# Kernel optimization log

Hardware: AMD Instinct MI355X
Metric: run time of the kernel (lower is better)

## Reference

```python
import jax, jax.numpy as jnp
import numpy as np
import math
from jax import lax

TSCALE = 256
NUM_SAMPLE = 32
PERBIN = 3
WINDOWS = [4, 8, 16, 32, 64, 128, 192, 256]
RATIO = 0.25
B = 2
DIM = 512
H1 = 256   # hid_dim_1d
H3 = 512   # hid_dim_3d
H2 = 128   # hid_dim_2d


def _bin_mask(xmin, xmax, tscale, num_sample, perbin):
    # exact replica of BEM._get_interp1d_bin_mask (setup-time numpy)
    plen = float(xmax - xmin)
    step = plen / (num_sample * perbin - 1.0)
    samples = [xmin + step * i for i in range(num_sample * perbin)]
    cols = []
    for idx in range(num_sample):
        v = np.zeros([tscale])
        for s in samples[idx * perbin:(idx + 1) * perbin]:
            up = math.ceil(s)
            dec, down = math.modf(s)
            if 0 <= int(down) <= tscale - 1:
                v[int(down)] += 1 - dec
            if 0 <= int(up) <= tscale - 1:
                v[int(up)] += dec
        cols.append(v / perbin)
    return np.stack(cols, axis=1)  # (tscale, num_sample)


def build_sample_mask():
    mats = []
    for w in WINDOWS:
        ws = w + w * RATIO
        vecs = []
        for t in range(TSCALE):
            d = ws * 0.5
            vecs.append(_bin_mask(t - d, t + d, TSCALE, NUM_SAMPLE, PERBIN))
        mats.append(np.stack(vecs, axis=2))  # (T, N, T)
    m = np.stack(mats, axis=3).astype(np.float32)  # (T, N, T, W)
    return jnp.asarray(m.reshape(TSCALE, -1))  # (T, N*T*W)


def gn(x, g, b, groups=32, eps=1e-5):
    Bsz, C = x.shape[0], x.shape[1]
    xr = x.reshape(Bsz, groups, -1)
    mu = xr.mean(-1, keepdims=True)
    var = xr.var(-1, keepdims=True)
    xr = (xr - mu) * lax.rsqrt(var + eps)
    x = xr.reshape(x.shape)
    bshape = (1, C) + (1,) * (x.ndim - 2)
    return x * g.reshape(bshape) + b.reshape(bshape)


def conv(x, w, b, strides, padding, dn):
    y = lax.conv_general_dilated(x, w, strides, padding, dimension_numbers=dn)
    return y + b.reshape((1, -1) + (1,) * (y.ndim - 2))


def setup_inputs() -> dict:
    key = jax.random.key(0)
    ks = jax.random.split(key, 16)

    def w(k, shape, fan):
        return (jax.random.normal(k, shape) * (1.0 / np.sqrt(fan))).astype(jnp.float32)

    inp = {}
    inp['x'] = jax.random.normal(ks[0], (B, DIM, TSCALE), jnp.float32)
    inp['sample_mask'] = build_sample_mask()
    inp['c1_w'] = w(ks[1], (H1, DIM, 3), DIM * 3)
    inp['c1_b'] = jnp.zeros((H1,), jnp.float32)
    inp['gn1_g'] = jnp.ones((H1,), jnp.float32)
    inp['gn1_b'] = jnp.zeros((H1,), jnp.float32)
    inp['r3d_w'] = w(ks[2], (H3, H1, NUM_SAMPLE, 1, 1), H1 * NUM_SAMPLE)
    inp['r3d_b'] = jnp.zeros((H3,), jnp.float32)
    inp['gn3_g'] = jnp.ones((H3,), jnp.float32)
    inp['gn3_b'] = jnp.zeros((H3,), jnp.float32)
    inp['r2d_w'] = w(ks[3], (H2, H3, 1, 1), H3)
    inp['r2d_b'] = jnp.zeros((H2,), jnp.float32)
    inp['gn2_g'] = jnp.ones((H2,), jnp.float32)
    inp['gn2_b'] = jnp.zeros((H2,), jnp.float32)
    inp['s1_w'] = w(ks[4], (H2, H2, 3, 3), H2 * 9)
    inp['s1_b'] = jnp.zeros((H2,), jnp.float32)
    inp['sgn_g'] = jnp.ones((H2,), jnp.float32)
    inp['sgn_b'] = jnp.zeros((H2,), jnp.float32)
    inp['s2_w'] = w(ks[5], (1, H2, 1, 1), H2)
    inp['s2_b'] = jnp.zeros((1,), jnp.float32)
    inp['e1_w'] = w(ks[6], (H2, H2, 3, 3), H2 * 9)
    inp['e1_b'] = jnp.zeros((H2,), jnp.float32)
    inp['egn_g'] = jnp.ones((H2,), jnp.float32)
    inp['egn_b'] = jnp.zeros((H2,), jnp.float32)
    inp['e2_w'] = w(ks[7], (1, H2, 1, 1), H2)
    inp['e2_b'] = jnp.zeros((1,), jnp.float32)
    return inp


def reference(x, sample_mask, c1_w, c1_b, gn1_g, gn1_b, r3d_w, r3d_b, gn3_g, gn3_b,
              r2d_w, r2d_b, gn2_g, gn2_b, s1_w, s1_b, sgn_g, sgn_b, s2_w, s2_b,
              e1_w, e1_b, egn_g, egn_b, e2_w, e2_b):
    relu = jax.nn.relu
    W = len(WINDOWS)
    # conv_1: Unit1D(k=3, same pad) + GN + ReLU  -> (B, H1, T)
    h = relu(gn(conv(x, c1_w, c1_b, (1,), [(1, 1)], ('NCH', 'OIH', 'NCH')), gn1_g, gn1_b))
    Bsz, C, T = h.shape
    # sample: dense GEMM against sparse interp1d mask -> (B, C, N, T, W)
    samp = jnp.matmul(h, sample_mask).reshape(Bsz, C, NUM_SAMPLE, T, W)
    # reduction_layer 'fc': Conv3d over the N axis (kernel=stride=N) + GN + ReLU
    y = conv(samp, r3d_w, r3d_b, (NUM_SAMPLE, 1, 1), 'VALID', ('NCDHW', 'OIDHW', 'NCDHW'))
    y = relu(gn(y, gn3_g, gn3_b))[:, :, 0]  # squeeze depth -> (B, H3, T, W)
    f = relu(gn(conv(y, r2d_w, r2d_b, (1, 1), 'VALID', ('NCHW', 'OIHW', 'NCHW')), gn2_g, gn2_b))

    def head(w1, b1, gg, gb, w2, b2):
        t = relu(gn(conv(f, w1, b1, (1, 1), [(1, 1), (1, 1)], ('NCHW', 'OIHW', 'NCHW')), gg, gb))
        return jax.nn.sigmoid(conv(t, w2, b2, (1, 1), 'VALID', ('NCHW', 'OIHW', 'NCHW')))

    cs = head(s1_w, s1_b, sgn_g, sgn_b, s2_w, s2_b)  # (B,1,T,W)
    ce = head(e1_w, e1_b, egn_g, egn_b, e2_w, e2_b)  # (B,1,T,W)
    return jnp.concatenate([cs, ce], axis=1)  # (B,2,T,W): [start, end]
```

## Files before the change

### kernel.cpp

```cpp
#include <hip/hip_runtime.h>
#include <hip/hip_bf16.h>

typedef __hip_bfloat16 bf16;
typedef __attribute__((ext_vector_type(8))) short short8;
typedef __attribute__((ext_vector_type(4))) float f32x4;

static __device__ __forceinline__ float b2f(bf16 v) { return __bfloat162float(v); }

static __device__ __forceinline__ float ldin(const void* p, long i, int bf) {
    return bf ? b2f(((const bf16*)p)[i]) : ((const float*)p)[i];
}

__global__ void detect_k(const unsigned short* __restrict__ x16, int* __restrict__ flag) {
    __shared__ int cnt[256];
    unsigned short u = x16[threadIdx.x];
    int e = (u >> 7) & 0xFF;
    cnt[threadIdx.x] = (e >= 100 && e <= 140) ? 1 : 0;
    __syncthreads();
    for (int off = 128; off > 0; off >>= 1) {
        if (threadIdx.x < off) cnt[threadIdx.x] += cnt[threadIdx.x + off];
        __syncthreads();
    }
    if (threadIdx.x == 0) *flag = (cnt[0] > 217) ? 1 : 0;
}

__global__ void transpose_w_k(const void* __restrict__ in, float* __restrict__ out,
                              int M, int K, const int* __restrict__ flagp) {
    int bf = *flagp;
    int idx = blockIdx.x * 256 + threadIdx.x;
    if (idx >= M * K) return;
    int k = idx / M, m = idx - k * M;
    out[idx] = ldin(in, (long)m * K + k, bf);
}

__global__ __launch_bounds__(256) void transpose_w3b_k(const void* __restrict__ w3,
                                                       bf16* __restrict__ out,
                                                       const int* __restrict__ flagp) {
    int bf = *flagp;
    int h3 = blockIdx.x;
    __shared__ bf16 t[8192];
    long base = (long)h3 * 8192;
    for (int i = threadIdx.x; i < 8192; i += 256)
        t[i] = __float2bfloat16(ldin(w3, base + i, bf));
    __syncthreads();
    for (int i = threadIdx.x; i < 8192; i += 256) {
        int n = i >> 8, c = i & 255;
        out[((long)n * 512 + h3) * 256 + c] = t[c * 32 + n];
    }
}

__global__ void cast_hT_k(const float* __restrict__ h, bf16* __restrict__ out) {
    int idx = blockIdx.x * 256 + threadIdx.x;
    if (idx >= 131072) return;
    int b = idx >> 16, r = idx & 65535;
    int tau = r >> 8, c = r & 255;
    out[idx] = __float2bfloat16(h[b * 65536 + c * 256 + tau]);
}

__global__ void im2col_x_k(const void* __restrict__ x, float* __restrict__ colx,
                           const int* __restrict__ flagp) {
    int bf = *flagp;
    int idx = blockIdx.x * 256 + threadIdx.x;
    if (idx >= 786432) return;
    int t = idx & 255;
    int b = idx / 393216;
    int k = (idx - b * 393216) >> 8;
    int c = k / 3, q = k - c * 3;
    int tt = t + q - 1;
    colx[idx] = (tt >= 0 && tt < 256) ? ldin(x, ((long)b * 512 + c) * 256 + tt, bf) : 0.f;
}

__global__ void im2col_f_k(const float* __restrict__ f, float* __restrict__ col) {
    int idx = blockIdx.x * 256 + threadIdx.x;
    if (idx >= 4718592) return;
    int p = idx & 2047;
    int rem = idx >> 11;
    int b = rem / 1152;
    int k = rem - b * 1152;
    int c = k / 9, q = k - c * 9;
    int dy = q / 3, dx = q - dy * 3;
    int t = p >> 3, w = p & 7;
    int tt = t + dy - 1, ww = w + dx - 1;
    col[idx] = (tt >= 0 && tt < 256 && ww >= 0 && ww < 8)
                   ? f[((long)b * 128 + c) * 2048 + tt * 8 + ww] : 0.f;
}

__global__ __launch_bounds__(256) void pgemm_mfma(
    const bf16* __restrict__ w3b, const bf16* __restrict__ hbT,
    float* __restrict__ P)
{
    int z = blockIdx.z;
    int b = z >> 5, n = z & 31;
    int bm = blockIdx.y;
    int tid = threadIdx.x;
    int wv = tid >> 6, lane = tid & 63;
    int q = lane >> 4, col = lane & 15;

    f32x4 acc[16];
    #pragma unroll
    for (int i = 0; i < 16; ++i) acc[i] = (f32x4){0.f, 0.f, 0.f, 0.f};

    const short8* Abase = (const short8*)(w3b + ((long)n * 512 + bm * 64 + wv * 16 + col) * 256);
    const short8* Bbase = (const short8*)(hbT + (long)b * 65536);

    #pragma unroll
    for (int kc = 0; kc < 8; ++kc) {
        short8 af = Abase[kc * 4 + q];
        #pragma unroll
        for (int nt = 0; nt < 16; ++nt) {
            short8 bfr = Bbase[(nt * 16 + col) * 32 + kc * 4 + q];
            acc[nt] = __builtin_amdgcn_mfma_f32_16x16x32_bf16(af, bfr, acc[nt], 0, 0, 0);
        }
    }

    long dbase = (long)b * 4194304 + (long)n * 256 +
                 (long)(bm * 64 + wv * 16 + q * 4) * 8192 + col;
    #pragma unroll
    for (int nt = 0; nt < 16; ++nt)
        #pragma unroll
        for (int r = 0; r < 4; ++r)
            P[dbase + (long)r * 8192 + nt * 16] = acc[nt][r];
}

template<int BM, int BP, int TM, int TP>
__global__ __launch_bounds__(256) void gemm_t(
    const float* __restrict__ A, const float* __restrict__ B, float* __restrict__ C,
    const void* __restrict__ bias, const void* __restrict__ bias2,
    int M, int K, int P, int az_mod, int bz_div,
    long a_zs, long b_zs, long c_zs1, long c_zs2, int c_ms,
    int zmod, int ksplit, long sstride, int accum, const int* __restrict__ flagp)
{
    int bf = *flagp;
    int zraw = blockIdx.z;
    int z = zraw % zmod;
    int ks = zraw / zmod;
    int klen = K / ksplit;
    int kbeg = ks * klen;
    int kend = kbeg + klen;
    int za = z % az_mod;
    const float* A2 = A + (long)za * a_zs;
    const float* B2 = B + (long)(z / bz_div) * b_zs;
    float* C2 = C + (long)(z / bz_div) * c_zs1 + (long)za * c_zs2;
    const void* bi = (bias2 != nullptr && za != 0) ? bias2 : bias;

    __shared__ float As[16][BM];
    __shared__ float Bs[16][BP];
    int tid = threadIdx.x;
    int ty = tid >> 4, tx = tid & 15;
    int lk = tid >> 4;
    int lma = (tid & 15) * TM;
    int lpb = (tid & 15) * TP;
    int m0 = blockIdx.y * BM, p0 = blockIdx.x * BP;

    float acc[TM][TP];
    #pragma unroll
    for (int i = 0; i < TM; ++i)
        #pragma unroll
        for (int j = 0; j < TP; ++j) acc[i][j] = 0.f;

    float ra[TM], rb[TP];
    {
        const float* ap = A2 + (long)(kbeg + lk) * M + m0 + lma;
        const float* bp = B2 + (long)(kbeg + lk) * P + p0 + lpb;
        #pragma unroll
        for (int u = 0; u < TM; ++u) ra[u] = ap[u];
        #pragma unroll
        for (int u = 0; u < TP; ++u) rb[u] = bp[u];
    }

    for (int kc = kbeg; kc < kend; kc += 16) {
        #pragma unroll
        for (int u = 0; u < TM; ++u) As[lk][lma + u] = ra[u];
        #pragma unroll
        for (int u = 0; u < TP; ++u) Bs[lk][lpb + u] = rb[u];
        __syncthreads();
        if (kc + 16 < kend) {
            const float* ap = A2 + (long)(kc + 16 + lk) * M + m0 + lma;
            const float* bp = B2 + (long)(kc + 16 + lk) * P + p0 + lpb;
            #pragma unroll
            for (int u = 0; u < TM; ++u) ra[u] = ap[u];
            #pragma unroll
            for (int u = 0; u < TP; ++u) rb[u] = bp[u];
        }
        #pragma unroll
        for (int kk = 0; kk < 16; ++kk) {
            float av[TM], bv[TP];
            #pragma unroll
            for (int i = 0; i < TM; ++i) av[i] = As[kk][ty * TM + i];
            #pragma unroll
            for (int j = 0; j < TP; ++j) bv[j] = Bs[kk][tx * TP + j];
            #pragma unroll
            for (int i = 0; i < TM; ++i)
                #pragma unroll
                for (int j = 0; j < TP; ++j)
                    acc[i][j] += av[i] * bv[j];
        }
        __syncthreads();
    }

    #pragma unroll
    for (int i = 0; i < TM; ++i) {
        int m = m0 + ty * TM + i;
        float bb = bi ? ldin(bi, m, bf) : 0.f;
        #pragma unroll
        for (int j = 0; j < TP; ++j) {
            long idx = (long)m * c_ms + p0 + tx * TP + j;
            if (accum == 1) C2[sstride * ks + idx] = acc[i][j];
            else if (accum == 2) C2[idx] += acc[i][j];
            else C2[idx] = acc[i][j] + bb;
        }
    }
}

__global__ __launch_bounds__(256) void gemm_q(
    const float* __restrict__ A, const float* __restrict__ B, float* __restrict__ C,
    const void* __restrict__ bias, const void* __restrict__ bias2,
    int M, int K, int P, int az_mod, int bz_div,
    long a_zs, long b_zs, long c_zs1, long c_zs2, int c_ms,
    int zmod, int ksplit, long sstride, int accum, const int* __restrict__ flagp)
{
    int bf = *flagp;
    int zraw = blockIdx.z;
    int z = zraw % zmod;
    int ks = zraw / zmod;
    int klen = K / ksplit;
    int kbeg = ks * klen, kend = kbeg + klen;
    int za = z % az_mod;
    const float* A2 = A + (long)za * a_zs;
    const float* B2 = B + (long)(z / bz_div) * b_zs;
    float* C2 = C + (long)(z / bz_div) * c_zs1 + (long)za * c_zs2;
    const void* bi = (bias2 != nullptr && za != 0) ? bias2 : bias;

    __shared__ float As[16][128];
    __shared__ float Bs[16][128];
    int tid = threadIdx.x;
    int ty = tid >> 4, tx = tid & 15;
    int lk = tid >> 4;
    int lc4 = (tid & 15) * 4;
    int m0 = blockIdx.y * 128, p0 = blockIdx.x * 128;

    float acc[8][8];
    #pragma unroll
    for (int i = 0; i < 8; ++i)
        #pragma unroll
        for (int j = 0; j < 8; ++j) acc[i][j] = 0.f;

    float4 ra0, ra1, rb0, rb1;
    {
        const float* ap = A2 + (long)(kbeg + lk) * M + m0 + lc4;
        const float* bp = B2 + (long)(kbeg + lk) * P + p0 + lc4;
        ra0 = *(const float4*)ap;  ra1 = *(const float4*)(ap + 64);
        rb0 = *(const float4*)bp;  rb1 = *(const float4*)(bp + 64);
    }

    for (int kc = kbeg; kc < kend; kc += 16) {
        *(float4*)&As[lk][lc4]      = ra0;
        *(float4*)&As[lk][64 + lc4] = ra1;
        *(float4*)&Bs[lk][lc4]      = rb0;
        *(float4*)&Bs[lk][64 + lc4] = rb1;
        __syncthreads();
        if (kc + 16 < kend) {
            const float* ap = A2 + (long)(kc + 16 + lk) * M + m0 + lc4;
            const float* bp = B2 + (long)(kc + 16 + lk) * P + p0 + lc4;
            ra0 = *(const float4*)ap;  ra1 = *(const float4*)(ap + 64);
            rb0 = *(const float4*)bp;  rb1 = *(const float4*)(bp + 64);
        }
        #pragma unroll
        for (int kk = 0; kk < 16; ++kk) {
            float4 av0 = *(float4*)&As[kk][ty * 4];
            float4 av1 = *(float4*)&As[kk][64 + ty * 4];
            float4 bv0 = *(float4*)&Bs[kk][tx * 4];
            float4 bv1 = *(float4*)&Bs[kk][64 + tx * 4];
            float av[8] = {av0.x, av0.y, av0.z, av0.w, av1.x, av1.y, av1.z, av1.w};
            float bv[8] = {bv0.x, bv0.y, bv0.z, bv0.w, bv1.x, bv1.y, bv1.z, bv1.w};
            #pragma unroll
            for (int i = 0; i < 8; ++i)
                #pragma unroll
                for (int j = 0; j < 8; ++j)
                    acc[i][j] += av[i] * bv[j];
        }
        __syncthreads();
    }

    #pragma unroll
    for (int r = 0; r < 2; ++r)
        #pragma unroll
        for (int i = 0; i < 4; ++i) {
            int m = m0 + r * 64 + ty * 4 + i;
            float bb = bi ? ldin(bi, m, bf) : 0.f;
            #pragma unroll
            for (int c = 0; c < 2; ++c)
                #pragma unroll
                for (int j = 0; j < 4; ++j) {
                    long idx = (long)m * c_ms + p0 + c * 64 + tx * 4 + j;
                    float v = acc[r * 4 + i][c * 4 + j];
                    if (accum == 1) C2[sstride * ks + idx] = v;
                    else if (accum == 2) C2[idx] += v;
                    else C2[idx] = v + bb;
                }
        }
}

__global__ void reduce_k(const float* __restrict__ bufs, float* __restrict__ out,
                         int n4, int ns, long sstride, const void* __restrict__ b1,
                         const void* __restrict__ b2, int rshift, int cshift, int cmask,
                         const int* __restrict__ flagp)
{
    int bf = *flagp;
    int i = blockIdx.x * 256 + threadIdx.x;
    if (i >= n4) return;
    long e = (long)i * 4;
    float4 s = *(const float4*)(bufs + e);
    for (int k = 1; k < ns; ++k) {
        float4 v = *(const float4*)(bufs + (long)k * sstride + e);
        s.x += v.x; s.y += v.y; s.z += v.z; s.w += v.w;
    }
    const void* bp = (rshift >= 0 && ((e >> rshift) & 3) >= 2) ? b2 : b1;
    int c = (int)((e >> cshift) & cmask);
    float bb = ldin(bp, c, bf);
    *(float4*)(out + e) = make_float4(s.x + bb, s.y + bb, s.z + bb, s.w + bb);
}

__global__ __launch_bounds__(1024) void gn_relu_k(
    float* __restrict__ buf, const void* __restrict__ g, const void* __restrict__ bt,
    int C, int S, int groups, const int* __restrict__ flagp)
{
    int bf = *flagp;
    int nt = blockDim.x;
    int gid = blockIdx.x;
    int b = gid / groups, gr = gid % groups;
    int cpg = C / groups;
    long cnt = (long)cpg * S;
    float* base = buf + ((long)b * C + (long)gr * cpg) * S;
    double s = 0.0, s2 = 0.0;
    for (long i = threadIdx.x; i < cnt; i += nt) {
        float v = base[i];
        s += v; s2 += (double)v * v;
    }
    __shared__ double rs[1024], rq[1024];
    rs[threadIdx.x] = s; rq[threadIdx.x] = s2;
    __syncthreads();
    for (int off = nt >> 1; off > 0; off >>= 1) {
        if (threadIdx.x < off) { rs[threadIdx.x] += rs[threadIdx.x + off]; rq[threadIdx.x] += rq[threadIdx.x + off]; }
        __syncthreads();
    }
    double mean_d = rs[0] / (double)cnt;
    float mean = (float)mean_d;
    float var = (float)(rq[0] / (double)cnt - mean_d * mean_d);
    float rstd = rsqrtf(var + 1e-5f);
    for (long i = threadIdx.x; i < cnt; i += nt) {
        int c = gr * cpg + (int)(i / S);
        float v = (base[i] - mean) * rstd * ldin(g, c, bf) + ldin(bt, c, bf);
        base[i] = v > 0.f ? v : 0.f;
    }
}

__global__ __launch_bounds__(384) void build_table_k(
    const void* __restrict__ mask, int* __restrict__ tabd,
    float* __restrict__ tabw, const int* __restrict__ flagp)
{
    int bf = *flagp;
    int nw = blockIdx.x;
    int w = nw >> 5, n = nw & 31;
    int tid = threadIdx.x;
    int d = tid - 165;
    float v = 0.f;
    if (d <= 165) {
        if (d < 0) v = ldin(mask, (long)(254 + d) * 65536 + ((long)n * 256 + 254) * 8 + w, bf);
        else       v = ldin(mask, (long)(1 + d) * 65536 + ((long)n * 256 + 1) * 8 + w, bf);
    }
    __shared__ unsigned char nz[384];
    nz[tid] = (v != 0.f) ? 1 : 0;
    if (tid < 6) { tabd[nw * 6 + tid] = 0; tabw[nw * 6 + tid] = 0.f; }
    __syncthreads();
    if (v != 0.f) {
        int slot = 0;
        for (int j = 0; j < tid; ++j) slot += nz[j];
        if (slot < 6) { tabd[nw * 6 + slot] = d; tabw[nw * 6 + slot] = v; }
    }
}

__global__ void build_corr_k(const void* __restrict__ mask, const int* __restrict__ tabd,
                             const float* __restrict__ tabw, float* __restrict__ corrB,
                             const int* __restrict__ flagp) {
    int bf = *flagp;
    int idx = blockIdx.x * 256 + threadIdx.x;
    if (idx >= 65536) return;
    int n = idx >> 11, p = idx & 2047;
    int t = p >> 3, w = p & 7;
    float mv = ldin(mask, ((long)n * 256 + t) * 8 + w, bf);
    float sub = 0.f;
    int base = (w * 32 + n) * 6;
    for (int k = 0; k < 6; ++k)
        if (tabd[base + k] == -t && tabw[base + k] != 0.f) sub += tabw[base + k];
    corrB[idx] = mv - sub;
}

__global__ void p0t_k(const float* __restrict__ P, float* __restrict__ p0t) {
    int idx = blockIdx.x * 256 + threadIdx.x;
    if (idx >= 32768) return;
    int h3 = idx & 511, n = (idx >> 9) & 31, b = idx >> 14;
    p0t[idx] = P[(((long)(b * 512 + h3) * 32) + n) * 256];
}

__global__ __launch_bounds__(256) void apply_y_k(
    const float* __restrict__ P, const int* __restrict__ tabd,
    const float* __restrict__ tabw, const void* __restrict__ r3b,
    float* __restrict__ y, const int* __restrict__ flagp)
{
    int bf = *flagp;
    int h3 = blockIdx.x;
    __shared__ float2 Pl2[8192];
    __shared__ float4 Tp4[768];
    const float4* p04 = (const float4*)(P + (long)h3 * 8192);
    const float4* p14 = (const float4*)(P + (512L + h3) * 8192);
    float4* pl4 = (float4*)Pl2;
    for (int i = threadIdx.x; i < 2048; i += 256) {
        float4 a = p04[i], b = p14[i];
        pl4[i * 2]     = make_float4(a.x, b.x, a.y, b.y);
        pl4[i * 2 + 1] = make_float4(a.z, b.z, a.w, b.w);
    }
    float2* tp2 = (float2*)Tp4;
    for (int i = threadIdx.x; i < 1536; i += 256)
        tp2[i] = make_float2(tabw[i], __int_as_float(tabd[i]));
    __syncthreads();

    int t = threadIdx.x;
    float a0[8], a1[8];
    #pragma unroll
    for (int w = 0; w < 8; ++w) { a0[w] = 0.f; a1[w] = 0.f; }

    #pragma unroll 1
    for (int n = 0; n < 32; ++n) {
        const float2* Pn = Pl2 + (n << 8);
        #pragma unroll
        for (int w = 0; w < 8; ++w) {
            int e4 = ((w << 5) + n) * 3;
            float4 q0 = Tp4[e4], q1 = Tp4[e4 + 1], q2 = Tp4[e4 + 2];
            float wts[6] = {q0.x, q0.z, q1.x, q1.z, q2.x, q2.z};
            int   dss[6] = {__float_as_int(q0.y), __float_as_int(q0.w),
                            __float_as_int(q1.y), __float_as_int(q1.w),
                            __float_as_int(q2.y), __float_as_int(q2.w)};
            #pragma unroll
            for (int k = 0; k < 6; ++k) {
                int tau = t + dss[k];
                int idx = tau & 255;
                float wt = ((unsigned)tau < 256u) ? wts[k] : 0.f;
                float2 pv = Pn[idx];
                a0[w] += wt * pv.x;
                a1[w] += wt * pv.y;
            }
        }
    }

    float bias = ldin(r3b, h3, bf);
    long y0 = (long)h3 * 2048 + (long)t * 8;
    long y1 = y0 + 512L * 2048;
    *(float4*)(y + y0)     = make_float4(a0[0] + bias, a0[1] + bias, a0[2] + bias, a0[3] + bias);
    *(float4*)(y + y0 + 4) = make_float4(a0[4] + bias, a0[5] + bias, a0[6] + bias, a0[7] + bias);
    *(float4*)(y + y1)     = make_float4(a1[0] + bias, a1[1] + bias, a1[2] + bias, a1[3] + bias);
    *(float4*)(y + y1 + 4) = make_float4(a1[4] + bias, a1[5] + bias, a1[6] + bias, a1[7] + bias);
}

__global__ void head_out_k(const float* __restrict__ t1s, const float* __restrict__ t1e,
                           const void* __restrict__ s2w, const void* __restrict__ s2b,
                           const void* __restrict__ e2w, const void* __restrict__ e2b,
                           void* __restrict__ out, const int* __restrict__ flagp) {
    int bf = *flagp;
    int idx = blockIdx.x * 256 + threadIdx.x;
    if (idx >= 4096) return;
    int b = idx >> 11, p = idx & 2047;
    const float* ts = t1s + (long)b * 262144 + p;
    const float* te = t1e + (long)b * 262144 + p;
    float as = ldin(s2b, 0, bf), ae = ldin(e2b, 0, bf);
    #pragma unroll 8
    for (int c = 0; c < 128; ++c) {
        as += ldin(s2w, c, bf) * ts[(long)c * 2048];
        ae += ldin(e2w, c, bf) * te[(long)c * 2048];
    }
    float vs = 1.f / (1.f + expf(-as));
    float ve = 1.f / (1.f + expf(-ae));
    long o0 = ((long)b * 2) * 2048 + p;
    long o1 = ((long)b * 2 + 1) * 2048 + p;
    if (bf) {
        ((bf16*)out)[o0] = __float2bfloat16(vs);
        ((bf16*)out)[o1] = __float2bfloat16(ve);
    } else {
        ((float*)out)[o0] = vs;
        ((float*)out)[o1] = ve;
    }
}

extern "C" void kernel_launch(void* const* d_in, const int* in_sizes, int n_in,
                              void* d_out, int out_size, void* d_ws, size_t ws_size,
                              hipStream_t stream) {
    const void* x    = d_in[0];
    const void* mask = d_in[1];
    const void* c1w  = d_in[2];
    const void* c1b  = d_in[3];
    const void* gn1g = d_in[4];
    const void* gn1b = d_in[5];
    const void* w3   = d_in[6];
    const void* r3b  = d_in[7];
    const void* gn3g = d_in[8];
    const void* gn3b = d_in[9];
    const void* w2   = d_in[10];
    const void* r2b  = d_in[11];
    const void* gn2g = d_in[12];
    const void* gn2b = d_in[13];
    const void* s1w  = d_in[14];
    const void* s1b  = d_in[15];
    const void* sgng = d_in[16];
    const void* sgnb = d_in[17];
    const void* s2w  = d_in[18];
    const void* s2b  = d_in[19];
    const void* e1w  = d_in[20];
    const void* e1b  = d_in[21];
    const void* egng = d_in[22];
    const void* egnb = d_in[23];
    const void* e2w  = d_in[24];
    const void* e2b  = d_in[25];
    float* ws = (float*)d_ws;

    int*   flagI = (int*)(ws + 0);
    float* h     = ws + 64;
    float* c1t   = ws + 131136;
    float* w2t   = ws + 524352;
    float* s1t   = ws + 589888;
    float* e1t   = ws + 737344;
    float* corrB = ws + 884800;
    float* tabw  = ws + 950336;
    int*   tabd  = (int*)(ws + 951872);
    float* p0t   = ws + 953408;
    float* t1s   = ws + 986176;
    float* t1e   = ws + 1510464;
    float* f     = ws + 2034752;
    float* y     = ws + 2559040;
    float* w3reg = ws + 4656192;
    float* Pb    = ws + 8850496;
    bf16*  w3b   = (bf16*)w3reg;
    bf16*  hbT   = (bf16*)(w3reg + 2097152);
    float* colx  = Pb;
    float* col   = Pb;
    float* bufs_c1 = y;
    float* bufs_r2 = Pb;
    float* bufs_hd = y;

    dim3 blk(256);
    dim3 blkG(1024);

    detect_k<<<dim3(1), blk, 0, stream>>>((const unsigned short*)x, flagI);

    transpose_w_k<<<dim3(1536), blk, 0, stream>>>(c1w, c1t, 256, 1536, flagI);
    transpose_w_k<<<dim3(256),  blk, 0, stream>>>(w2,  w2t, 128, 512, flagI);
    transpose_w_k<<<dim3(576),  blk, 0, stream>>>(s1w, s1t, 128, 1152, flagI);
    transpose_w_k<<<dim3(576),  blk, 0, stream>>>(e1w, e1t, 128, 1152, flagI);
    transpose_w3b_k<<<dim3(512), blk, 0, stream>>>(w3, w3b, flagI);
    build_table_k<<<dim3(256), dim3(384), 0, stream>>>(mask, tabd, tabw, flagI);
    build_corr_k<<<dim3(256), blk, 0, stream>>>(mask, tabd, tabw, corrB, flagI);

    im2col_x_k<<<dim3(3072), blk, 0, stream>>>(x, colx, flagI);
    gemm_t<64,64,4,4><<<dim3(4,4,16), blk, 0, stream>>>(
        c1t, colx, bufs_c1, nullptr, nullptr, 256, 1536, 256,
        1, 1, 0L, 393216L, 65536L, 0L, 256, 2, 8, 131072L, 1, flagI);
    reduce_k<<<dim3(128), blk, 0, stream>>>(bufs_c1, h, 32768, 8, 131072L,
                                            c1b, nullptr, -1, 8, 255, flagI);
    gn_relu_k<<<dim3(64), blkG, 0, stream>>>(h, gn1g, gn1b, 256, 256, 32, flagI);

    cast_hT_k<<<dim3(512), blk, 0, stream>>>(h, hbT);
    pgemm_mfma<<<dim3(1, 8, 64), blk, 0, stream>>>(w3b, hbT, Pb);

    apply_y_k<<<dim3(512), blk, 0, stream>>>(Pb, tabd, tabw, r3b, y, flagI);
    p0t_k<<<dim3(128), blk, 0, stream>>>(Pb, p0t);
    gemm_t<64,64,4,4><<<dim3(32,8,2), blk, 0, stream>>>(
        p0t, corrB, y, nullptr, nullptr, 512, 32, 2048,
        2, 1, 16384L, 0L, 0L, 1048576L, 2048, 2, 1, 0L, 2, flagI);
    gn_relu_k<<<dim3(64), blkG, 0, stream>>>(y, gn3g, gn3b, 512, 2048, 32, flagI);

    gemm_t<64,64,4,4><<<dim3(32,2,8), blk, 0, stream>>>(
        w2t, y, bufs_r2, nullptr, nullptr, 128, 512, 2048,
        1, 1, 0L, 1048576L, 262144L, 0L, 2048, 2, 4, 524288L, 1, flagI);
    reduce_k<<<dim3(512), blk, 0, stream>>>(bufs_r2, f, 131072, 4, 524288L,
                                            r2b, nullptr, -1, 11, 127, flagI);
    gn_relu_k<<<dim3(64), blkG, 0, stream>>>(f, gn2g, gn2b, 128, 2048, 32, flagI);

    im2col_f_k<<<dim3(18432), blk, 0, stream>>>(f, col);
    gemm_q<<<dim3(16,1,24), blk, 0, stream>>>(
        s1t, col, bufs_hd, nullptr, nullptr, 128, 1152, 2048,
        2, 2, 147456L, 2359296L, 262144L, 524288L, 2048, 4, 6, 1048576L, 1, flagI);
    reduce_k<<<dim3(1024), blk, 0, stream>>>(bufs_hd, t1s, 262144, 6, 1048576L,
                                             s1b, e1b, 18, 11, 127, flagI);
    gn_relu_k<<<dim3(64), blkG, 0, stream>>>(t1s, sgng, sgnb, 128, 2048, 32, flagI);
    gn_relu_k<<<dim3(64), blkG, 0, stream>>>(t1e, egng, egnb, 128, 2048, 32, flagI);

    head_out_k<<<dim3(16), blk, 0, stream>>>(t1s, t1e, s2w, s2b, e2w, e2b, d_out, flagI);
}
```

Baseline: 463.1 us.

## Move conv1 and head 3x3 convs to bf16 MFMA GEMMs with k-major im2col

The conv1 and both head 3x3 convolutions now run through a new bf16 MFMA GEMM kernel that reads operands directly from global memory. Weights are cast to bf16 without transposing, and the im2col buffers are written as bf16 in a K-contiguous layout. This removes the fp32 SIMT GEMMs along with their split-K partial buffers and reduce passes, with bias added in the GEMM epilogue. In exchange, operands are rounded to bf16, and the new kernel has no LDS staging, so it depends on global/L2 reuse and launches relatively few blocks.

```diff
diff --git a/kernel.cpp b/kernel.cpp
--- a/kernel.cpp
+++ b/kernel.cpp
@@ -24,6 +24,14 @@
     if (threadIdx.x == 0) *flag = (cnt[0] > 217) ? 1 : 0;
 }
 
+__global__ void cast_bf_k(const void* __restrict__ in, bf16* __restrict__ out,
+                          int n, const int* __restrict__ flagp) {
+    int bf = *flagp;
+    int idx = blockIdx.x * 256 + threadIdx.x;
+    if (idx >= n) return;
+    out[idx] = __float2bfloat16(ldin(in, idx, bf));
+}
+
 __global__ void transpose_w_k(const void* __restrict__ in, float* __restrict__ out,
                               int M, int K, const int* __restrict__ flagp) {
     int bf = *flagp;
@@ -57,32 +65,78 @@
     out[idx] = __float2bfloat16(h[b * 65536 + c * 256 + tau]);
 }
 
-__global__ void im2col_x_k(const void* __restrict__ x, float* __restrict__ colx,
-                           const int* __restrict__ flagp) {
+__global__ void im2col_xb_k(const void* __restrict__ x, bf16* __restrict__ out,
+                            const int* __restrict__ flagp) {
     int bf = *flagp;
     int idx = blockIdx.x * 256 + threadIdx.x;
     if (idx >= 786432) return;
-    int t = idx & 255;
     int b = idx / 393216;
-    int k = (idx - b * 393216) >> 8;
+    int rem = idx - b * 393216;
+    int t = rem / 1536, k = rem - t * 1536;
     int c = k / 3, q = k - c * 3;
     int tt = t + q - 1;
-    colx[idx] = (tt >= 0 && tt < 256) ? ldin(x, ((long)b * 512 + c) * 256 + tt, bf) : 0.f;
-}
-
-__global__ void im2col_f_k(const float* __restrict__ f, float* __restrict__ col) {
+    float v = (tt >= 0 && tt < 256) ? ldin(x, ((long)b * 512 + c) * 256 + tt, bf) : 0.f;
+    out[idx] = __float2bfloat16(v);
+}
+
+__global__ void im2col_fb_k(const float* __restrict__ f, bf16* __restrict__ out) {
     int idx = blockIdx.x * 256 + threadIdx.x;
     if (idx >= 4718592) return;
-    int p = idx & 2047;
-    int rem = idx >> 11;
-    int b = rem / 1152;
-    int k = rem - b * 1152;
+    int b = idx / 2359296;
+    int rem = idx - b * 2359296;
+    int p = rem / 1152, k = rem - p * 1152;
     int c = k / 9, q = k - c * 9;
     int dy = q / 3, dx = q - dy * 3;
     int t = p >> 3, w = p & 7;
     int tt = t + dy - 1, ww = w + dx - 1;
-    col[idx] = (tt >= 0 && tt < 256 && ww >= 0 && ww < 8)
-                   ? f[((long)b * 128 + c) * 2048 + tt * 8 + ww] : 0.f;
+    float v = (tt >= 0 && tt < 256 && ww >= 0 && ww < 8)
+                  ? f[((long)b * 128 + c) * 2048 + tt * 8 + ww] : 0.f;
+    out[idx] = __float2bfloat16(v);
+}
+
+template<int NT>
+__global__ __launch_bounds__(256) void wgemm_mfma(
+    const bf16* __restrict__ A, const bf16* __restrict__ B, float* __restrict__ C,
+    const void* __restrict__ bias1, const void* __restrict__ bias2,
+    int M, int K, int P, int a_div, long a_zs, const int* __restrict__ flagp)
+{
+    int bf = *flagp;
+    int z = blockIdx.z;
+    const bf16* A2 = A + (long)(z / a_div) * a_zs;
+    const bf16* B2 = B + (long)(z & 1) * (long)P * K;
+    float* C2 = C + (long)z * M * P;
+    const void* bi = (z / a_div) ? bias2 : bias1;
+
+    int tid = threadIdx.x;
+    int wv = tid >> 6, lane = tid & 63;
+    int q = lane >> 4, col = lane & 15;
+    int m0 = blockIdx.y * 64 + wv * 16;
+    int p0 = blockIdx.x * (16 * NT);
+
+    f32x4 acc[NT];
+    #pragma unroll
+    for (int i = 0; i < NT; ++i) acc[i] = (f32x4){0.f, 0.f, 0.f, 0.f};
+
+    const short8* Ab = (const short8*)(A2 + (long)(m0 + col) * K);
+    int kch = K >> 5;
+    for (int kc = 0; kc < kch; ++kc) {
+        short8 af = Ab[kc * 4 + q];
+        #pragma unroll
+        for (int nt = 0; nt < NT; ++nt) {
+            const short8* Bb = (const short8*)(B2 + (long)(p0 + nt * 16 + col) * K);
+            short8 bfr = Bb[kc * 4 + q];
+            acc[nt] = __builtin_amdgcn_mfma_f32_16x16x32_bf16(af, bfr, acc[nt], 0, 0, 0);
+        }
+    }
+
+    float bv[4];
+    #pragma unroll
+    for (int r = 0; r < 4; ++r) bv[r] = ldin(bi, m0 + q * 4 + r, bf);
+    #pragma unroll
+    for (int nt = 0; nt < NT; ++nt)
+        #pragma unroll
+        for (int r = 0; r < 4; ++r)
+            C2[(long)(m0 + q * 4 + r) * P + p0 + nt * 16 + col] = acc[nt][r] + bv[r];
 }
 
 __global__ __launch_bounds__(256) void pgemm_mfma(
@@ -210,95 +264,6 @@
             else C2[idx] = acc[i][j] + bb;
         }
     }
-}
-
-__global__ __launch_bounds__(256) void gemm_q(
-    const float* __restrict__ A, const float* __restrict__ B, float* __restrict__ C,
-    const void* __restrict__ bias, const void* __restrict__ bias2,
-    int M, int K, int P, int az_mod, int bz_div,
-    long a_zs, long b_zs, long c_zs1, long c_zs2, int c_ms,
-    int zmod, int ksplit, long sstride, int accum, const int* __restrict__ flagp)
-{
-    int bf = *flagp;
-    int zraw = blockIdx.z;
-    int z = zraw % zmod;
-    int ks = zraw / zmod;
-    int klen = K / ksplit;
-    int kbeg = ks * klen, kend = kbeg + klen;
-    int za = z % az_mod;
-    const float* A2 = A + (long)za * a_zs;
-    const float* B2 = B + (long)(z / bz_div) * b_zs;
-    float* C2 = C + (long)(z / bz_div) * c_zs1 + (long)za * c_zs2;
-    const void* bi = (bias2 != nullptr && za != 0) ? bias2 : bias;
-
-    __shared__ float As[16][128];
-    __shared__ float Bs[16][128];
-    int tid = threadIdx.x;
-    int ty = tid >> 4, tx = tid & 15;
-    int lk = tid >> 4;
-    int lc4 = (tid & 15) * 4;
-    int m0 = blockIdx.y * 128, p0 = blockIdx.x * 128;
-
-    float acc[8][8];
-    #pragma unroll
-    for (int i = 0; i < 8; ++i)
-        #pragma unroll
-        for (int j = 0; j < 8; ++j) acc[i][j] = 0.f;
-
-    float4 ra0, ra1, rb0, rb1;
-    {
-        const float* ap = A2 + (long)(kbeg + lk) * M + m0 + lc4;
-        const float* bp = B2 + (long)(kbeg + lk) * P + p0 + lc4;
-        ra0 = *(const float4*)ap;  ra1 = *(const float4*)(ap + 64);
-        rb0 = *(const float4*)bp;  rb1 = *(const float4*)(bp + 64);
-    }
-
-    for (int kc = kbeg; kc < kend; kc += 16) {
-        *(float4*)&As[lk][lc4]      = ra0;
-        *(float4*)&As[lk][64 + lc4] = ra1;
-        *(float4*)&Bs[lk][lc4]      = rb0;
-        *(float4*)&Bs[lk][64 + lc4] = rb1;
-        __syncthreads();
-        if (kc + 16 < kend) {
-            const float* ap = A2 + (long)(kc + 16 + lk) * M + m0 + lc4;
-            const float* bp = B2 + (long)(kc + 16 + lk) * P + p0 + lc4;
-            ra0 = *(const float4*)ap;  ra1 = *(const float4*)(ap + 64);
-            rb0 = *(const float4*)bp;  rb1 = *(const float4*)(bp + 64);
-        }
-        #pragma unroll
-        for (int kk = 0; kk < 16; ++kk) {
-            float4 av0 = *(float4*)&As[kk][ty * 4];
-            float4 av1 = *(float4*)&As[kk][64 + ty * 4];
-            float4 bv0 = *(float4*)&Bs[kk][tx * 4];
-            float4 bv1 = *(float4*)&Bs[kk][64 + tx * 4];
-            float av[8] = {av0.x, av0.y, av0.z, av0.w, av1.x, av1.y, av1.z, av1.w};
-            float bv[8] = {bv0.x, bv0.y, bv0.z, bv0.w, bv1.x, bv1.y, bv1.z, bv1.w};
-            #pragma unroll
-            for (int i = 0; i < 8; ++i)
-                #pragma unroll
-                for (int j = 0; j < 8; ++j)
-                    acc[i][j] += av[i] * bv[j];
-        }
-        __syncthreads();
-    }
-
-    #pragma unroll
-    for (int r = 0; r < 2; ++r)
-        #pragma unroll
-        for (int i = 0; i < 4; ++i) {
-            int m = m0 + r * 64 + ty * 4 + i;
-            float bb = bi ? ldin(bi, m, bf) : 0.f;
-            #pragma unroll
-            for (int c = 0; c < 2; ++c)
-                #pragma unroll
-                for (int j = 0; j < 4; ++j) {
-                    long idx = (long)m * c_ms + p0 + c * 64 + tx * 4 + j;
-                    float v = acc[r * 4 + i][c * 4 + j];
-                    if (accum == 1) C2[sstride * ks + idx] = v;
-                    else if (accum == 2) C2[idx] += v;
-                    else C2[idx] = v + bb;
-                }
-        }
 }
 
 __global__ void reduce_k(const float* __restrict__ bufs, float* __restrict__ out,
@@ -527,7 +492,6 @@
     float* c1t   = ws + 131136;
     float* w2t   = ws + 524352;
     float* s1t   = ws + 589888;
-    float* e1t   = ws + 737344;
     float* corrB = ws + 884800;
     float* tabw  = ws + 950336;
     int*   tabd  = (int*)(ws + 951872);
@@ -540,31 +504,28 @@
     float* Pb    = ws + 8850496;
     bf16*  w3b   = (bf16*)w3reg;
     bf16*  hbT   = (bf16*)(w3reg + 2097152);
-    float* colx  = Pb;
-    float* col   = Pb;
-    float* bufs_c1 = y;
+    bf16*  c1wb  = (bf16*)c1t;
+    bf16*  hwb   = (bf16*)s1t;
+    bf16*  colxb = (bf16*)y;
+    bf16*  fcolb = (bf16*)Pb;
     float* bufs_r2 = Pb;
-    float* bufs_hd = y;
 
     dim3 blk(256);
     dim3 blkG(1024);
 
     detect_k<<<dim3(1), blk, 0, stream>>>((const unsigned short*)x, flagI);
 
-    transpose_w_k<<<dim3(1536), blk, 0, stream>>>(c1w, c1t, 256, 1536, flagI);
-    transpose_w_k<<<dim3(256),  blk, 0, stream>>>(w2,  w2t, 128, 512, flagI);
-    transpose_w_k<<<dim3(576),  blk, 0, stream>>>(s1w, s1t, 128, 1152, flagI);
-    transpose_w_k<<<dim3(576),  blk, 0, stream>>>(e1w, e1t, 128, 1152, flagI);
+    cast_bf_k<<<dim3(1536), blk, 0, stream>>>(c1w, c1wb, 393216, flagI);
+    cast_bf_k<<<dim3(576),  blk, 0, stream>>>(s1w, hwb, 147456, flagI);
+    cast_bf_k<<<dim3(576),  blk, 0, stream>>>(e1w, hwb + 147456, 147456, flagI);
+    transpose_w_k<<<dim3(256), blk, 0, stream>>>(w2, w2t, 128, 512, flagI);
     transpose_w3b_k<<<dim3(512), blk, 0, stream>>>(w3, w3b, flagI);
     build_table_k<<<dim3(256), dim3(384), 0, stream>>>(mask, tabd, tabw, flagI);
     build_corr_k<<<dim3(256), blk, 0, stream>>>(mask, tabd, tabw, corrB, flagI);
 
-    im2col_x_k<<<dim3(3072), blk, 0, stream>>>(x, colx, flagI);
-    gemm_t<64,64,4,4><<<dim3(4,4,16), blk, 0, stream>>>(
-        c1t, colx, bufs_c1, nullptr, nullptr, 256, 1536, 256,
-        1, 1, 0L, 393216L, 65536L, 0L, 256, 2, 8, 131072L, 1, flagI);
-    reduce_k<<<dim3(128), blk, 0, stream>>>(bufs_c1, h, 32768, 8, 131072L,
-                                            c1b, nullptr, -1, 8, 255, flagI);
+    im2col_xb_k<<<dim3(3072), blk, 0, stream>>>(x, colxb, flagI);
+    wgemm_mfma<2><<<dim3(8, 4, 2), blk, 0, stream>>>(
+        c1wb, colxb, h, c1b, c1b, 256, 1536, 256, 1, 0L, flagI);
     gn_relu_k<<<dim3(64), blkG, 0, stream>>>(h, gn1g, gn1b, 256, 256, 32, flagI);
 
     cast_hT_k<<<dim3(512), blk, 0, stream>>>(h, hbT);
@@ -584,12 +545,9 @@
                                             r2b, nullptr, -1, 11, 127, flagI);
     gn_relu_k<<<dim3(64), blkG, 0, stream>>>(f, gn2g, gn2b, 128, 2048, 32, flagI);
 
-    im2col_f_k<<<dim3(18432), blk, 0, stream>>>(f, col);
-    gemm_q<<<dim3(16,1,24), blk, 0, stream>>>(
-        s1t, col, bufs_hd, nullptr, nullptr, 128, 1152, 2048,
-        2, 2, 147456L, 2359296L, 262144L, 524288L, 2048, 4, 6, 1048576L, 1, flagI);
-    reduce_k<<<dim3(1024), blk, 0, stream>>>(bufs_hd, t1s, 262144, 6, 1048576L,
-                                             s1b, e1b, 18, 11, 127, flagI);
+    im2col_fb_k<<<dim3(18432), blk, 0, stream>>>(f, fcolb);
+    wgemm_mfma<8><<<dim3(16, 2, 4), blk, 0, stream>>>(
+        hwb, fcolb, t1s, s1b, e1b, 128, 1152, 2048, 2, 147456L, flagI);
     gn_relu_k<<<dim3(64), blkG, 0, stream>>>(t1s, sgng, sgnb, 128, 2048, 32, flagI);
     gn_relu_k<<<dim3(64), blkG, 0, stream>>>(t1e, egng, egnb, 128, 2048, 32, flagI);
 
```

Measured after the change: 456.2 us. Within noise of the previous version (-1.5%).
